# Optimization experiments

Hardware: AMD Instinct MI355X
Metric: run time of the kernel (lower is better)

Reference implementation:

```python
import math
import jax, jax.numpy as jnp
import numpy as np

B, L, HID = 2, 2048, 2048
H = 16
D = HID // H  # 128
EPS = 1e-6
ROPE_BASE = 10000.0
BETA_MIN, BETA_MAX = 0.8, 0.9995


def _rope_cache(seq_len, dim):
    half = dim // 2
    inv_freq = 1.0 / (ROPE_BASE ** (jnp.arange(half, dtype=jnp.float32) / float(half)))
    t = jnp.arange(seq_len, dtype=jnp.float32)
    freqs = t[:, None] * inv_freq[None, :]  # [L, half]
    return jnp.cos(freqs), jnp.sin(freqs)


def _apply_rope(x, cos, sin):
    # x: [B, H, L, D]; cos/sin: [L, D//2]
    half = x.shape[-1] // 2
    xe, xo = x[..., :half], x[..., half:]
    c = cos[None, None]
    s = sin[None, None]
    return jnp.concatenate([xe * c - xo * s, xe * s + xo * c], axis=-1)


def setup_inputs() -> dict:
    key = jax.random.key(0)
    ks = jax.random.split(key, 6)
    sc = 1.0 / math.sqrt(HID)  # ~ xavier scale
    return {
        "x": jax.random.normal(ks[0], (B, L, HID), jnp.float32),
        "Wq": jax.random.normal(ks[1], (HID, HID), jnp.float32) * sc,
        "Wk": jax.random.normal(ks[2], (HID, HID), jnp.float32) * sc,
        "Wv": jax.random.normal(ks[3], (HID, HID), jnp.float32) * sc,
        "Wg": jax.random.normal(ks[4], (HID, H), jnp.float32) * sc,
        "bg": jnp.full((H,), math.log(0.98 / (1.0 - 0.98)), jnp.float32),
        "Wo": jax.random.normal(ks[5], (HID, HID), jnp.float32) * sc,
        "bo": jnp.zeros((HID,), jnp.float32),
    }


def _deltanet(x, Wq, Wk, Wv, Wg, bg, Wo, bo):
    Bb, Ll, _ = x.shape
    split = lambda t: t.reshape(Bb, Ll, H, D).transpose(0, 2, 1, 3)  # [B,H,L,D]
    q = split(x @ Wq)
    k = split(x @ Wk)
    v = split(x @ Wv)

    cos, sin = _rope_cache(Ll, D)
    q = _apply_rope(q, cos, sin)
    k = _apply_rope(k, cos, sin)

    beta = jax.nn.sigmoid(x @ Wg + bg)                # [B,L,H]
    beta = jnp.clip(beta, BETA_MIN, BETA_MAX).transpose(0, 2, 1)  # [B,H,L]

    phi_q = jax.nn.elu(q) + 1.0
    phi_k = jax.nn.elu(k) + 1.0

    # time-major for scan
    pq = phi_q.transpose(2, 0, 1, 3)  # [L,B,H,D]
    pk = phi_k.transpose(2, 0, 1, 3)
    vt = v.transpose(2, 0, 1, 3)
    bt = beta.transpose(2, 0, 1)      # [L,B,H]

    S0 = jnp.zeros((Bb, H, D, D), jnp.float32)
    z0 = jnp.zeros((Bb, H, D), jnp.float32)

    def step(carry, inp):
        S, z = carry
        pq_t, pk_t, v_t, b_t = inp
        S = S * b_t[..., None, None] + pk_t[..., :, None] * v_t[..., None, :]
        z = z * b_t[..., None] + pk_t
        numer = jnp.einsum('bhd,bhde->bhe', pq_t, S)
        denom = jnp.sum(pq_t * z, axis=-1, keepdims=True) + EPS
        return (S, z), numer / denom

    (_, _), y = jax.lax.scan(step, (S0, z0), (pq, pk, vt, bt))  # y: [L,B,H,D]
    y = y.transpose(1, 0, 2, 3).reshape(Bb, Ll, HID)  # [B,L,H*D]
    return y @ Wo + bo


def reference(x, Wq, Wk, Wv, Wg, bg, Wo, bo):
    return _deltanet(x, Wq, Wk, Wv, Wg, bg, Wo, bo)
```

## Files before the change

### kernel.cpp

```cpp
#include <hip/hip_runtime.h>


typedef __attribute__((ext_vector_type(8))) short short8;
typedef __attribute__((ext_vector_type(4))) float f32x4;

__device__ __forceinline__ unsigned short f2bf(float f) {
  unsigned u = __float_as_uint(f);
  u += 0x7fffu + ((u >> 16) & 1u);
  return (unsigned short)(u >> 16);
}
__device__ __forceinline__ float bf2f(unsigned short s) {
  return __uint_as_float(((unsigned)s) << 16);
}
__device__ __forceinline__ float phi_elu1(float x) {
  return x > 0.f ? x + 1.f : expf(x);
}
__device__ __forceinline__ void gl_lds16(const void* g, void* l) {
  __builtin_amdgcn_global_load_lds(
      (const __attribute__((address_space(1))) void*)g,
      (__attribute__((address_space(3))) void*)l, 16, 0, 0);
}

__global__ __launch_bounds__(256)
void k_cast(const float* __restrict__ x, unsigned short* __restrict__ xb) {
  int i = (blockIdx.x * 256 + threadIdx.x) * 4;
  float4 f = *(const float4*)(x + i);
  uint2 p;
  p.x = (unsigned)f2bf(f.x) | ((unsigned)f2bf(f.y) << 16);
  p.y = (unsigned)f2bf(f.z) | ((unsigned)f2bf(f.w) << 16);
  *(uint2*)(xb + i) = p;
}

__global__ __launch_bounds__(256)
void k_transw(const float* __restrict__ Wq, const float* __restrict__ Wk,
              const float* __restrict__ Wv, const float* __restrict__ Wo,
              unsigned short* __restrict__ Wt, unsigned short* __restrict__ Wot) {
  const int z = blockIdx.z;
  const float* W = (z == 0) ? Wq : (z == 1) ? Wk : (z == 2) ? Wv : Wo;
  unsigned short* out = (z < 3) ? (Wt + (size_t)z * 2048 * 2048) : Wot;
  __shared__ float tile[64][65];
  const int n0 = blockIdx.x * 64;
  const int k0 = blockIdx.y * 64;
  const int tx = threadIdx.x & 63;
  const int ty = threadIdx.x >> 6;
#pragma unroll
  for (int rl = 0; rl < 16; ++rl) {
    int kk = rl * 4 + ty;
    tile[kk][tx] = W[(size_t)(k0 + kk) * 2048 + n0 + tx];
  }
  __syncthreads();
#pragma unroll
  for (int rl = 0; rl < 16; ++rl) {
    int nn = rl * 4 + ty;
    out[(size_t)(n0 + nn) * 2048 + k0 + tx] = f2bf(tile[tx][nn]);
  }
}

__global__ __launch_bounds__(256)
void k_transg16(const float* __restrict__ Wg, unsigned short* __restrict__ Wgt16) {
  int idx = blockIdx.x * 256 + threadIdx.x;
  int h = idx >> 11, k = idx & 2047;
  Wgt16[idx] = f2bf(Wg[k * 16 + h]);
}

__global__ __launch_bounds__(256)
void k_betaW(const unsigned short* __restrict__ xb, const unsigned short* __restrict__ Wgt16,
             const float* __restrict__ bg, float* __restrict__ beta) {
  const int w = threadIdx.x >> 6;
  const int lane = threadIdx.x & 63;
  const int m = blockIdx.x * 4 + w;
  const int h = lane & 15, kq = lane >> 4;
  const unsigned short* xr = xb + (size_t)m * 2048 + kq * 512;
  const unsigned short* wr = Wgt16 + (size_t)h * 2048 + kq * 512;
  float acc = 0.f;
#pragma unroll 8
  for (int i = 0; i < 64; ++i) {
    short8 xv = *(const short8*)(xr + i * 8);
    short8 wv = *(const short8*)(wr + i * 8);
#pragma unroll
    for (int j = 0; j < 8; ++j)
      acc = fmaf(bf2f((unsigned short)xv[j]), bf2f((unsigned short)wv[j]), acc);
  }
  acc += __shfl_xor(acc, 16, 64);
  acc += __shfl_xor(acc, 32, 64);
  if (lane < 16) {
    float v = acc + bg[h];
    float bv = 1.f / (1.f + expf(-v));
    beta[(size_t)m * 16 + h] = fminf(fmaxf(bv, 0.8f), 0.9995f);
  }
}

template <bool OUT_BF16, bool ADD_BIAS>
__global__ __launch_bounds__(256)
void k_gemm(const unsigned short* __restrict__ A, const unsigned short* __restrict__ Bt,
            void* __restrict__ Cptr, const float* __restrict__ bias,
            int M, int N, int K, int ldA, int ldC) {
  __shared__ __align__(16) unsigned short As[128][32];
  __shared__ __align__(16) unsigned short Bs[128][32];
  const int tid = threadIdx.x;
  const int n0 = blockIdx.x * 128;
  const int m0 = blockIdx.y * 128;
  const int lane = tid & 63;
  const int w = tid >> 6;
  const int wm = w >> 1, wn = w & 1;
  const int q = lane >> 4, r = lane & 15;

  const int srow = w * 32 + (lane >> 2);
  const int skc = (lane & 3) * 8;

  f32x4 acc[4][4];
#pragma unroll
  for (int i = 0; i < 4; ++i)
#pragma unroll
    for (int j = 0; j < 4; ++j) acc[i][j] = (f32x4){0.f, 0.f, 0.f, 0.f};

  const unsigned short* Ap = A + (size_t)(m0 + srow) * ldA + skc;
  const unsigned short* Ap2 = Ap + (size_t)16 * ldA;
  const unsigned short* Bp = Bt + (size_t)(n0 + srow) * K + skc;
  const unsigned short* Bp2 = Bp + (size_t)16 * K;

  for (int kt = 0; kt < K; kt += 32) {
    __syncthreads();
    gl_lds16(Ap + kt, &As[srow][skc]);
    gl_lds16(Ap2 + kt, &As[srow + 16][skc]);
    gl_lds16(Bp + kt, &Bs[srow][skc]);
    gl_lds16(Bp2 + kt, &Bs[srow + 16][skc]);
    __syncthreads();
    short8 af[4], bfr[4];
#pragma unroll
    for (int i = 0; i < 4; ++i)
      af[i] = *(const short8*)&As[wm * 64 + i * 16 + r][q * 8];
#pragma unroll
    for (int j = 0; j < 4; ++j)
      bfr[j] = *(const short8*)&Bs[wn * 64 + j * 16 + r][q * 8];
#pragma unroll
    for (int i = 0; i < 4; ++i)
#pragma unroll
      for (int j = 0; j < 4; ++j)
        acc[i][j] = __builtin_amdgcn_mfma_f32_16x16x32_bf16(af[i], bfr[j], acc[i][j], 0, 0, 0);
  }
#pragma unroll
  for (int i = 0; i < 4; ++i) {
#pragma unroll
    for (int j = 0; j < 4; ++j) {
#pragma unroll
      for (int rr = 0; rr < 4; ++rr) {
        int mi = m0 + wm * 64 + i * 16 + q * 4 + rr;
        int ni = n0 + wn * 64 + j * 16 + r;
        float val = acc[i][j][rr];
        if (ADD_BIAS) val += bias[ni];
        if (OUT_BF16)
          ((unsigned short*)Cptr)[(size_t)mi * ldC + ni] = f2bf(val);
        else
          ((float*)Cptr)[(size_t)mi * ldC + ni] = val;
      }
    }
  }
}

__global__ __launch_bounds__(256)
void k_prep(const unsigned short* __restrict__ qkv, const float* __restrict__ beta,
            unsigned short* __restrict__ Qt, unsigned short* __restrict__ Ktg,
            unsigned short* __restrict__ Ag, float* __restrict__ gch) {
  const int ch = blockIdx.x;
  const int bh = blockIdx.y;
  const int b = bh >> 4, h = bh & 15;
  const int tid = threadIdx.x;
  const int t0 = ch * 64;

  __shared__ float Gs[64];
  __shared__ unsigned short Qs[64][136];
  __shared__ unsigned short Ks[64][136];

  if (tid < 64) {
    float bb = beta[((size_t)(b * 2048 + t0 + tid)) * 16 + h];
#pragma unroll
    for (int off = 1; off < 64; off <<= 1) {
      float o = __shfl_up(bb, off, 64);
      if (tid >= off) bb *= o;
    }
    Gs[tid] = bb;
    if (tid == 63) gch[bh * 32 + ch] = bb;
  }
  __syncthreads();

  const int dgl = tid & 7;
  float invf[8];
#pragma unroll
  for (int j = 0; j < 8; ++j)
    invf[j] = expf((float)(dgl * 8 + j) * -0.14391156831212787f);

  int s = tid >> 3;
#pragma unroll
  for (int rep = 0; rep < 2; ++rep, s += 32) {
    size_t row = ((size_t)(b * 2048 + t0 + s)) * 6144 + (size_t)h * 128;
    short8 qlo = *(const short8*)(qkv + row + dgl * 8);
    short8 qhi = *(const short8*)(qkv + row + 64 + dgl * 8);
    short8 klo = *(const short8*)(qkv + row + 2048 + dgl * 8);
    short8 khi = *(const short8*)(qkv + row + 2048 + 64 + dgl * 8);
    float g = Gs[s];
    float ig = 1.f / g;
    float tg = (float)(t0 + s);
    short8 oql, oqh, okl, okh;
#pragma unroll
    for (int j = 0; j < 8; ++j) {
      float sn, cs;
      __sincosf(tg * invf[j], &sn, &cs);
      float qe = bf2f((unsigned short)qlo[j]), qo = bf2f((unsigned short)qhi[j]);
      float a0 = qe * cs - qo * sn, a1 = qe * sn + qo * cs;
      oql[j] = (short)f2bf(phi_elu1(a0) * g);
      oqh[j] = (short)f2bf(phi_elu1(a1) * g);
      float ke = bf2f((unsigned short)klo[j]), ko = bf2f((unsigned short)khi[j]);
      a0 = ke * cs - ko * sn;
      a1 = ke * sn + ko * cs;
      okl[j] = (short)f2bf(phi_elu1(a0) * ig);
      okh[j] = (short)f2bf(phi_elu1(a1) * ig);
    }
    size_t qbase = (((size_t)bh * 32 + ch) * 64 + s) * 128;
    *(short8*)(Qt + qbase + dgl * 8) = oql;
    *(short8*)(Qt + qbase + 64 + dgl * 8) = oqh;
    *(short8*)&Qs[s][dgl * 8] = oql;
    *(short8*)&Qs[s][64 + dgl * 8] = oqh;
    *(short8*)&Ks[s][dgl * 8] = okl;
    *(short8*)&Ks[s][64 + dgl * 8] = okh;
  }
  __syncthreads();

  {
    const int d = tid >> 1, sh = tid & 1;
    unsigned pk[16];
#pragma unroll
    for (int i = 0; i < 16; ++i)
      pk[i] = (unsigned)Ks[sh * 32 + 2 * i][d] | ((unsigned)Ks[sh * 32 + 2 * i + 1][d] << 16);
    unsigned short* kr = Ktg + ((size_t)bh * 32 + ch) * 8192 + (size_t)d * 64 + sh * 32;
#pragma unroll
    for (int i = 0; i < 4; ++i)
      *(uint4*)(kr + i * 8) = *(uint4*)&pk[i * 4];
  }

  {
    const int lane = tid & 63;
    const int w = tid >> 6;
    const int q = lane >> 4, r = lane & 15;
    f32x4 acc[4];
#pragma unroll
    for (int nt = 0; nt < 4; ++nt) acc[nt] = (f32x4){0.f, 0.f, 0.f, 0.f};
#pragma unroll
    for (int kk = 0; kk < 4; ++kk) {
      short8 af = *(const short8*)&Qs[w * 16 + r][kk * 32 + q * 8];
#pragma unroll
      for (int nt = 0; nt < 4; ++nt) {
        short8 bf = *(const short8*)&Ks[nt * 16 + r][kk * 32 + q * 8];
        acc[nt] = __builtin_amdgcn_mfma_f32_16x16x32_bf16(af, bf, acc[nt], 0, 0, 0);
      }
    }
    unsigned short* Agp = Ag + ((size_t)bh * 32 + ch) * 4096;
#pragma unroll
    for (int nt = 0; nt < 4; ++nt) {
#pragma unroll
      for (int rr = 0; rr < 4; ++rr) {
        int t_l = w * 16 + q * 4 + rr;
        int s_l = nt * 16 + r;
        float val = (s_l <= t_l) ? acc[nt][rr] : 0.f;
        Agp[t_l * 64 + s_l] = f2bf(val);
      }
    }
  }
}

__global__ __launch_bounds__(256)
void k_scan(const unsigned short* __restrict__ Qt, const unsigned short* __restrict__ Ktg,
            const unsigned short* __restrict__ Ag, const unsigned short* __restrict__ qkv,
            const float* __restrict__ gch, float* __restrict__ numer,
            float* __restrict__ invd) {
  const int eb = blockIdx.x;
  const int bh = blockIdx.y;
  const int b = bh >> 4, h = bh & 15;
  const int tid = threadIdx.x;
  const int lane = tid & 63;
  const int w = tid >> 6;
  const int q = lane >> 4, r = lane & 15;
  const int e0 = eb * 16;

  __shared__ unsigned short Qs[64][136];
  __shared__ unsigned short Kts[128][72];
  __shared__ unsigned short As[64][72];
  __shared__ unsigned short Vt[16][72];
  __shared__ unsigned short SbT[16][136];

  f32x4 S_acc[2];
  S_acc[0] = (f32x4){0.f, 0.f, 0.f, 0.f};
  S_acc[1] = (f32x4){0.f, 0.f, 0.f, 0.f};

  for (int ch = 0; ch < 32; ++ch) {
    __syncthreads();
    {
      const unsigned short* Qg = Qt + ((size_t)bh * 32 + ch) * 8192;
#pragma unroll
      for (int i = 0; i < 4; ++i) {
        int c = tid + i * 256;
        int ss = c >> 4, dg = c & 15;
        *(int4*)&Qs[ss][dg * 8] = *(const int4*)(Qg + ss * 128 + dg * 8);
      }
      const unsigned short* Kg = Ktg + ((size_t)bh * 32 + ch) * 8192;
#pragma unroll
      for (int i = 0; i < 4; ++i) {
        int c = tid + i * 256;
        int d = c >> 3, sg = c & 7;
        *(int4*)&Kts[d][sg * 8] = *(const int4*)(Kg + d * 64 + sg * 8);
      }
      const unsigned short* Agp = Ag + ((size_t)bh * 32 + ch) * 4096;
#pragma unroll
      for (int i = 0; i < 2; ++i) {
        int c = tid + i * 256;
        int t_l = c >> 3, sg = c & 7;
        *(int4*)&As[t_l][sg * 8] = *(const int4*)(Agp + t_l * 64 + sg * 8);
      }
      if (eb < 8) {
        int ss = tid >> 2, e4 = tid & 3;
        const unsigned short* vp =
            qkv + ((size_t)(b * 2048 + ch * 64 + ss)) * 6144 + 4096 + h * 128 + e0 + e4 * 4;
        uint2 vv = *(const uint2*)vp;
        const unsigned short* pv = (const unsigned short*)&vv;
#pragma unroll
        for (int j = 0; j < 4; ++j) Vt[e4 * 4 + j][ss] = pv[j];
      } else {
        int e = tid >> 4, s4 = (tid & 15) * 4;
#pragma unroll
        for (int j = 0; j < 4; ++j) Vt[e][s4 + j] = (e == 0) ? (unsigned short)0x3F80 : (unsigned short)0;
      }
#pragma unroll
      for (int i = 0; i < 2; ++i)
#pragma unroll
        for (int rr = 0; rr < 4; ++rr)
          SbT[r][(2 * w + i) * 16 + q * 4 + rr] = f2bf(S_acc[i][rr]);
    }
    __syncthreads();

    const float gc = gch[bh * 32 + ch];

    f32x4 nacc = (f32x4){0.f, 0.f, 0.f, 0.f};
#pragma unroll
    for (int kk = 0; kk < 4; ++kk) {
      short8 af = *(const short8*)&Qs[w * 16 + r][kk * 32 + q * 8];
      short8 bf = *(const short8*)&SbT[r][kk * 32 + q * 8];
      nacc = __builtin_amdgcn_mfma_f32_16x16x32_bf16(af, bf, nacc, 0, 0, 0);
    }
    short8 vf[2];
#pragma unroll
    for (int kk = 0; kk < 2; ++kk) {
      vf[kk] = *(const short8*)&Vt[r][kk * 32 + q * 8];
      short8 af = *(const short8*)&As[w * 16 + r][kk * 32 + q * 8];
      nacc = __builtin_amdgcn_mfma_f32_16x16x32_bf16(af, vf[kk], nacc, 0, 0, 0);
    }
#pragma unroll
    for (int rr = 0; rr < 4; ++rr) {
      int t_l = w * 16 + q * 4 + rr;
      size_t m = (size_t)b * 2048 + ch * 64 + t_l;
      if (eb < 8)
        numer[m * 2048 + h * 128 + e0 + r] = nacc[rr];
      else if (r == 0)
        invd[m * 16 + h] = 1.f / (nacc[rr] + 1e-6f);
    }

#pragma unroll
    for (int i = 0; i < 2; ++i) {
#pragma unroll
      for (int kk = 0; kk < 2; ++kk) {
        short8 af = *(const short8*)&Kts[(2 * w + i) * 16 + r][kk * 32 + q * 8];
        S_acc[i] = __builtin_amdgcn_mfma_f32_16x16x32_bf16(af, vf[kk], S_acc[i], 0, 0, 0);
      }
#pragma unroll
      for (int rr = 0; rr < 4; ++rr) S_acc[i][rr] *= gc;
    }
  }
}

__global__ __launch_bounds__(256)
void k_scale(const float* __restrict__ numer, const float* __restrict__ invd,
             unsigned short* __restrict__ nb) {
  int base = (blockIdx.x * 256 + threadIdx.x) * 8;
  int m = base >> 11;
  int h = (base & 2047) >> 7;
  float sc = invd[(size_t)m * 16 + h];
  float4 a = *(const float4*)(numer + base);
  float4 b = *(const float4*)(numer + base + 4);
  uint2 p0, p1;
  p0.x = (unsigned)f2bf(a.x * sc) | ((unsigned)f2bf(a.y * sc) << 16);
  p0.y = (unsigned)f2bf(a.z * sc) | ((unsigned)f2bf(a.w * sc) << 16);
  p1.x = (unsigned)f2bf(b.x * sc) | ((unsigned)f2bf(b.y * sc) << 16);
  p1.y = (unsigned)f2bf(b.z * sc) | ((unsigned)f2bf(b.w * sc) << 16);
  *(uint2*)(nb + base) = p0;
  *(uint2*)(nb + base + 4) = p1;
}

extern "C" void kernel_launch(void* const* d_in, const int* in_sizes, int n_in,
                              void* d_out, int out_size, void* d_ws, size_t ws_size,
                              hipStream_t stream) {
  const float* x  = (const float*)d_in[0];
  const float* Wq = (const float*)d_in[1];
  const float* Wk = (const float*)d_in[2];
  const float* Wv = (const float*)d_in[3];
  const float* Wg = (const float*)d_in[4];
  const float* bg = (const float*)d_in[5];
  const float* Wo = (const float*)d_in[6];
  const float* bo = (const float*)d_in[7];

  char* ws = (char*)d_ws;
  unsigned short* xb    = (unsigned short*)(ws);
  unsigned short* Qt    = (unsigned short*)(ws);
  unsigned short* numerb= (unsigned short*)(ws);
  unsigned short* Wt    = (unsigned short*)(ws + 16777216);
  unsigned short* Ktg   = (unsigned short*)(ws + 16777216);
  unsigned short* Ag    = (unsigned short*)(ws + 33554432);
  unsigned short* Wot   = (unsigned short*)(ws + 41943040);
  unsigned short* qkvb  = (unsigned short*)(ws + 50331648);
  float*          beta  = (float*)(ws + 100663296);
  float*          invd  = (float*)(ws + 100925440);
  float*          numer = (float*)(ws + 101187584);
  unsigned short* Wgt16 = (unsigned short*)(ws + 101187584);
  float*          gch   = (float*)d_out;

  k_cast<<<8192, 256, 0, stream>>>(x, xb);
  k_transw<<<dim3(32, 32, 4), 256, 0, stream>>>(Wq, Wk, Wv, Wo, Wt, Wot);
  k_transg16<<<128, 256, 0, stream>>>(Wg, Wgt16);
  k_gemm<true, false><<<dim3(48, 32), 256, 0, stream>>>(
      xb, Wt, qkvb, nullptr, 4096, 6144, 2048, 2048, 6144);
  k_betaW<<<1024, 256, 0, stream>>>(xb, Wgt16, bg, beta);
  k_prep<<<dim3(32, 32), 256, 0, stream>>>(qkvb, beta, Qt, Ktg, Ag, gch);
  k_scan<<<dim3(9, 32), 256, 0, stream>>>(Qt, Ktg, Ag, qkvb, gch, numer, invd);
  k_scale<<<4096, 256, 0, stream>>>(numer, invd, numerb);
  k_gemm<false, true><<<dim3(16, 32), 256, 0, stream>>>(
      numerb, Wot, d_out, bo, 4096, 2048, 2048, 2048, 2048);
}
```

Before: 477.6 us.

## Fuse denominator into scan, widen GEMM K-tile with swizzled LDS, merge Wg transpose

The chunked scan now keeps the running key-sum z in shared memory and computes the normaliser inside each block. The output is written directly as scaled bf16, which removes the ninth block column, the fp32 numerator round-trip and the separate scale kernel. The GEMM loads 64-wide K tiles into XOR-swizzled LDS, halving the number of barrier pairs per K and aiming to avoid bank conflicts. The Wg transpose is folded into the weight-transpose launch as an extra z slice. Every scan block now redundantly recomputes the denominator and z, and the larger LDS tiles may reduce GEMM occupancy.

```diff
diff --git a/kernel.cpp b/kernel.cpp
--- a/kernel.cpp
+++ b/kernel.cpp
@@ -34,8 +34,20 @@
 __global__ __launch_bounds__(256)
 void k_transw(const float* __restrict__ Wq, const float* __restrict__ Wk,
               const float* __restrict__ Wv, const float* __restrict__ Wo,
-              unsigned short* __restrict__ Wt, unsigned short* __restrict__ Wot) {
+              const float* __restrict__ Wg,
+              unsigned short* __restrict__ Wt, unsigned short* __restrict__ Wot,
+              unsigned short* __restrict__ Wgt16) {
   const int z = blockIdx.z;
+  if (z == 4) {
+    if (blockIdx.y != 0) return;
+    int idx = blockIdx.x * 256 + threadIdx.x;
+    int h = idx >> 9, k4 = (idx & 511) * 4;
+    uint2 p;
+    p.x = (unsigned)f2bf(Wg[(k4 + 0) * 16 + h]) | ((unsigned)f2bf(Wg[(k4 + 1) * 16 + h]) << 16);
+    p.y = (unsigned)f2bf(Wg[(k4 + 2) * 16 + h]) | ((unsigned)f2bf(Wg[(k4 + 3) * 16 + h]) << 16);
+    *(uint2*)(Wgt16 + (size_t)h * 2048 + k4) = p;
+    return;
+  }
   const float* W = (z == 0) ? Wq : (z == 1) ? Wk : (z == 2) ? Wv : Wo;
   unsigned short* out = (z < 3) ? (Wt + (size_t)z * 2048 * 2048) : Wot;
   __shared__ float tile[64][65];
@@ -54,13 +66,6 @@
     int nn = rl * 4 + ty;
     out[(size_t)(n0 + nn) * 2048 + k0 + tx] = f2bf(tile[tx][nn]);
   }
-}
-
-__global__ __launch_bounds__(256)
-void k_transg16(const float* __restrict__ Wg, unsigned short* __restrict__ Wgt16) {
-  int idx = blockIdx.x * 256 + threadIdx.x;
-  int h = idx >> 11, k = idx & 2047;
-  Wgt16[idx] = f2bf(Wg[k * 16 + h]);
 }
 
 __global__ __launch_bounds__(256)
@@ -95,8 +100,8 @@
 void k_gemm(const unsigned short* __restrict__ A, const unsigned short* __restrict__ Bt,
             void* __restrict__ Cptr, const float* __restrict__ bias,
             int M, int N, int K, int ldA, int ldC) {
-  __shared__ __align__(16) unsigned short As[128][32];
-  __shared__ __align__(16) unsigned short Bs[128][32];
+  __shared__ __align__(16) unsigned short As[128][64];
+  __shared__ __align__(16) unsigned short Bs[128][64];
   const int tid = threadIdx.x;
   const int n0 = blockIdx.x * 128;
   const int m0 = blockIdx.y * 128;
@@ -105,8 +110,8 @@
   const int wm = w >> 1, wn = w & 1;
   const int q = lane >> 4, r = lane & 15;
 
-  const int srow = w * 32 + (lane >> 2);
-  const int skc = (lane & 3) * 8;
+  const int srow0 = w * 8 + (lane >> 3);
+  const int scol = ((lane & 7) ^ ((lane >> 3) & 7)) * 8;
 
   f32x4 acc[4][4];
 #pragma unroll
@@ -114,30 +119,37 @@
 #pragma unroll
     for (int j = 0; j < 4; ++j) acc[i][j] = (f32x4){0.f, 0.f, 0.f, 0.f};
 
-  const unsigned short* Ap = A + (size_t)(m0 + srow) * ldA + skc;
-  const unsigned short* Ap2 = Ap + (size_t)16 * ldA;
-  const unsigned short* Bp = Bt + (size_t)(n0 + srow) * K + skc;
-  const unsigned short* Bp2 = Bp + (size_t)16 * K;
-
-  for (int kt = 0; kt < K; kt += 32) {
+  const unsigned short* A0 = A + (size_t)(m0 + srow0) * ldA + scol;
+  const unsigned short* B0 = Bt + (size_t)(n0 + srow0) * K + scol;
+  unsigned short* lA = &As[srow0][(lane & 7) * 8];
+  unsigned short* lB = &Bs[srow0][(lane & 7) * 8];
+
+  const int rsw = r & 7;
+
+  for (int kt = 0; kt < K; kt += 64) {
     __syncthreads();
-    gl_lds16(Ap + kt, &As[srow][skc]);
-    gl_lds16(Ap2 + kt, &As[srow + 16][skc]);
-    gl_lds16(Bp + kt, &Bs[srow][skc]);
-    gl_lds16(Bp2 + kt, &Bs[srow + 16][skc]);
+#pragma unroll
+    for (int i = 0; i < 4; ++i) {
+      gl_lds16(A0 + (size_t)i * 32 * ldA + kt, lA + i * 2048);
+      gl_lds16(B0 + (size_t)i * 32 * K + kt, lB + i * 2048);
+    }
     __syncthreads();
-    short8 af[4], bfr[4];
-#pragma unroll
-    for (int i = 0; i < 4; ++i)
-      af[i] = *(const short8*)&As[wm * 64 + i * 16 + r][q * 8];
-#pragma unroll
-    for (int j = 0; j < 4; ++j)
-      bfr[j] = *(const short8*)&Bs[wn * 64 + j * 16 + r][q * 8];
-#pragma unroll
-    for (int i = 0; i < 4; ++i)
+#pragma unroll
+    for (int kk = 0; kk < 2; ++kk) {
+      const int ps = ((kk * 4 + q) ^ rsw) * 8;
+      short8 af[4], bfr[4];
+#pragma unroll
+      for (int i = 0; i < 4; ++i)
+        af[i] = *(const short8*)&As[wm * 64 + i * 16 + r][ps];
 #pragma unroll
       for (int j = 0; j < 4; ++j)
-        acc[i][j] = __builtin_amdgcn_mfma_f32_16x16x32_bf16(af[i], bfr[j], acc[i][j], 0, 0, 0);
+        bfr[j] = *(const short8*)&Bs[wn * 64 + j * 16 + r][ps];
+#pragma unroll
+      for (int i = 0; i < 4; ++i)
+#pragma unroll
+        for (int j = 0; j < 4; ++j)
+          acc[i][j] = __builtin_amdgcn_mfma_f32_16x16x32_bf16(af[i], bfr[j], acc[i][j], 0, 0, 0);
+    }
   }
 #pragma unroll
   for (int i = 0; i < 4; ++i) {
@@ -271,8 +283,7 @@
 __global__ __launch_bounds__(256)
 void k_scan(const unsigned short* __restrict__ Qt, const unsigned short* __restrict__ Ktg,
             const unsigned short* __restrict__ Ag, const unsigned short* __restrict__ qkv,
-            const float* __restrict__ gch, float* __restrict__ numer,
-            float* __restrict__ invd) {
+            const float* __restrict__ gch, unsigned short* __restrict__ numerb) {
   const int eb = blockIdx.x;
   const int bh = blockIdx.y;
   const int b = bh >> 4, h = bh & 15;
@@ -287,12 +298,15 @@
   __shared__ unsigned short As[64][72];
   __shared__ unsigned short Vt[16][72];
   __shared__ unsigned short SbT[16][136];
+  __shared__ __align__(16) float zbuf[2][128];
 
   f32x4 S_acc[2];
   S_acc[0] = (f32x4){0.f, 0.f, 0.f, 0.f};
   S_acc[1] = (f32x4){0.f, 0.f, 0.f, 0.f};
+  if (tid < 128) zbuf[0][tid] = 0.f;
 
   for (int ch = 0; ch < 32; ++ch) {
+    const int cur = ch & 1, nxt = cur ^ 1;
     __syncthreads();
     {
       const unsigned short* Qg = Qt + ((size_t)bh * 32 + ch) * 8192;
@@ -316,7 +330,7 @@
         int t_l = c >> 3, sg = c & 7;
         *(int4*)&As[t_l][sg * 8] = *(const int4*)(Agp + t_l * 64 + sg * 8);
       }
-      if (eb < 8) {
+      {
         int ss = tid >> 2, e4 = tid & 3;
         const unsigned short* vp =
             qkv + ((size_t)(b * 2048 + ch * 64 + ss)) * 6144 + 4096 + h * 128 + e0 + e4 * 4;
@@ -324,10 +338,6 @@
         const unsigned short* pv = (const unsigned short*)&vv;
 #pragma unroll
         for (int j = 0; j < 4; ++j) Vt[e4 * 4 + j][ss] = pv[j];
-      } else {
-        int e = tid >> 4, s4 = (tid & 15) * 4;
-#pragma unroll
-        for (int j = 0; j < 4; ++j) Vt[e][s4 + j] = (e == 0) ? (unsigned short)0x3F80 : (unsigned short)0;
       }
 #pragma unroll
       for (int i = 0; i < 2; ++i)
@@ -340,11 +350,23 @@
     const float gc = gch[bh * 32 + ch];
 
     f32x4 nacc = (f32x4){0.f, 0.f, 0.f, 0.f};
+    float dsum = 0.f;
 #pragma unroll
     for (int kk = 0; kk < 4; ++kk) {
       short8 af = *(const short8*)&Qs[w * 16 + r][kk * 32 + q * 8];
       short8 bf = *(const short8*)&SbT[r][kk * 32 + q * 8];
       nacc = __builtin_amdgcn_mfma_f32_16x16x32_bf16(af, bf, nacc, 0, 0, 0);
+      const float* zp = &zbuf[cur][kk * 32 + q * 8];
+      float4 z0a = *(const float4*)zp;
+      float4 z0b = *(const float4*)(zp + 4);
+      dsum = fmaf(bf2f((unsigned short)af[0]), z0a.x, dsum);
+      dsum = fmaf(bf2f((unsigned short)af[1]), z0a.y, dsum);
+      dsum = fmaf(bf2f((unsigned short)af[2]), z0a.z, dsum);
+      dsum = fmaf(bf2f((unsigned short)af[3]), z0a.w, dsum);
+      dsum = fmaf(bf2f((unsigned short)af[4]), z0b.x, dsum);
+      dsum = fmaf(bf2f((unsigned short)af[5]), z0b.y, dsum);
+      dsum = fmaf(bf2f((unsigned short)af[6]), z0b.z, dsum);
+      dsum = fmaf(bf2f((unsigned short)af[7]), z0b.w, dsum);
     }
     short8 vf[2];
 #pragma unroll
@@ -352,15 +374,32 @@
       vf[kk] = *(const short8*)&Vt[r][kk * 32 + q * 8];
       short8 af = *(const short8*)&As[w * 16 + r][kk * 32 + q * 8];
       nacc = __builtin_amdgcn_mfma_f32_16x16x32_bf16(af, vf[kk], nacc, 0, 0, 0);
-    }
+#pragma unroll
+      for (int j = 0; j < 8; ++j) dsum += bf2f((unsigned short)af[j]);
+    }
+    dsum += __shfl_xor(dsum, 16, 64);
+    dsum += __shfl_xor(dsum, 32, 64);
+    float inv = 1.f / (dsum + 1e-6f);
 #pragma unroll
     for (int rr = 0; rr < 4; ++rr) {
+      float inv_r = __shfl(inv, q * 4 + rr, 64);
       int t_l = w * 16 + q * 4 + rr;
       size_t m = (size_t)b * 2048 + ch * 64 + t_l;
-      if (eb < 8)
-        numer[m * 2048 + h * 128 + e0 + r] = nacc[rr];
-      else if (r == 0)
-        invd[m * 16 + h] = 1.f / (nacc[rr] + 1e-6f);
+      numerb[m * 2048 + h * 128 + e0 + r] = f2bf(nacc[rr] * inv_r);
+    }
+
+    {
+      int d = tid >> 1, half = tid & 1;
+      const unsigned short* kp = &Kts[d][half * 32];
+      float zs = 0.f;
+#pragma unroll
+      for (int i = 0; i < 4; ++i) {
+        short8 kv = *(const short8*)(kp + i * 8);
+#pragma unroll
+        for (int j = 0; j < 8; ++j) zs += bf2f((unsigned short)kv[j]);
+      }
+      zs += __shfl_xor(zs, 1, 64);
+      if (half == 0) zbuf[nxt][d] = gc * (zbuf[cur][d] + zs);
     }
 
 #pragma unroll
@@ -374,24 +413,6 @@
       for (int rr = 0; rr < 4; ++rr) S_acc[i][rr] *= gc;
     }
   }
-}
-
-__global__ __launch_bounds__(256)
-void k_scale(const float* __restrict__ numer, const float* __restrict__ invd,
-             unsigned short* __restrict__ nb) {
-  int base = (blockIdx.x * 256 + threadIdx.x) * 8;
-  int m = base >> 11;
-  int h = (base & 2047) >> 7;
-  float sc = invd[(size_t)m * 16 + h];
-  float4 a = *(const float4*)(numer + base);
-  float4 b = *(const float4*)(numer + base + 4);
-  uint2 p0, p1;
-  p0.x = (unsigned)f2bf(a.x * sc) | ((unsigned)f2bf(a.y * sc) << 16);
-  p0.y = (unsigned)f2bf(a.z * sc) | ((unsigned)f2bf(a.w * sc) << 16);
-  p1.x = (unsigned)f2bf(b.x * sc) | ((unsigned)f2bf(b.y * sc) << 16);
-  p1.y = (unsigned)f2bf(b.z * sc) | ((unsigned)f2bf(b.w * sc) << 16);
-  *(uint2*)(nb + base) = p0;
-  *(uint2*)(nb + base + 4) = p1;
 }
 
 extern "C" void kernel_launch(void* const* d_in, const int* in_sizes, int n_in,
@@ -409,27 +430,23 @@
   char* ws = (char*)d_ws;
   unsigned short* xb    = (unsigned short*)(ws);
   unsigned short* Qt    = (unsigned short*)(ws);
-  unsigned short* numerb= (unsigned short*)(ws);
   unsigned short* Wt    = (unsigned short*)(ws + 16777216);
   unsigned short* Ktg   = (unsigned short*)(ws + 16777216);
   unsigned short* Ag    = (unsigned short*)(ws + 33554432);
   unsigned short* Wot   = (unsigned short*)(ws + 41943040);
   unsigned short* qkvb  = (unsigned short*)(ws + 50331648);
   float*          beta  = (float*)(ws + 100663296);
-  float*          invd  = (float*)(ws + 100925440);
-  float*          numer = (float*)(ws + 101187584);
   unsigned short* Wgt16 = (unsigned short*)(ws + 101187584);
+  unsigned short* numerb= (unsigned short*)(ws + 101187584);
   float*          gch   = (float*)d_out;
 
   k_cast<<<8192, 256, 0, stream>>>(x, xb);
-  k_transw<<<dim3(32, 32, 4), 256, 0, stream>>>(Wq, Wk, Wv, Wo, Wt, Wot);
-  k_transg16<<<128, 256, 0, stream>>>(Wg, Wgt16);
+  k_transw<<<dim3(32, 32, 5), 256, 0, stream>>>(Wq, Wk, Wv, Wo, Wg, Wt, Wot, Wgt16);
   k_gemm<true, false><<<dim3(48, 32), 256, 0, stream>>>(
       xb, Wt, qkvb, nullptr, 4096, 6144, 2048, 2048, 6144);
   k_betaW<<<1024, 256, 0, stream>>>(xb, Wgt16, bg, beta);
   k_prep<<<dim3(32, 32), 256, 0, stream>>>(qkvb, beta, Qt, Ktg, Ag, gch);
-  k_scan<<<dim3(9, 32), 256, 0, stream>>>(Qt, Ktg, Ag, qkvb, gch, numer, invd);
-  k_scale<<<4096, 256, 0, stream>>>(numer, invd, numerb);
+  k_scan<<<dim3(8, 32), 256, 0, stream>>>(Qt, Ktg, Ag, qkvb, gch, numerb);
   k_gemm<false, true><<<dim3(16, 32), 256, 0, stream>>>(
       numerb, Wot, d_out, bo, 4096, 2048, 2048, 2048, 2048);
 }
```

Measured after the change: 435.3 us. 8.9% less time.
